# Optimization experiments

Hardware: AMD Instinct MI355X
Metric: run time of the kernel (lower is better)

Reference implementation:

```python
import jax, jax.numpy as jnp
import numpy as np

G, NPG, C, H, F, L = 256, 128, 16, 128, 128, 3
N = G * NPG          # 32768 nodes
E = 524288           # 16 edges per node on average
REG, REG_C = 0.01, 0.01
LN_EPS = 1e-5


def setup_inputs() -> dict:
    key = jax.random.key(0)
    ks = jax.random.split(key, 20)
    x = jax.random.normal(ks[0], (N, F), dtype=jnp.float32)
    # edges kept within each graph so dense pooling matches to_dense_batch semantics
    epg = E // G
    offs = jnp.repeat(jnp.arange(G, dtype=jnp.int64) * NPG, epg)
    src = jax.random.randint(ks[1], (E,), 0, NPG, dtype=jnp.int64) + offs
    tgt = jax.random.randint(ks[2], (E,), 0, NPG, dtype=jnp.int64) + offs
    edge_index = jnp.stack([src, tgt])
    mask_breaks = jax.random.bernoulli(ks[3], 0.5, (E,))
    s = jax.random.uniform(ks[4], (N, C), dtype=jnp.float32)
    batch = jnp.repeat(jnp.arange(G, dtype=jnp.int64), NPG)
    sc = 1.0 / np.sqrt(H)
    Wn = jax.random.normal(ks[5], (L, H, H), dtype=jnp.float32) * sc
    bn_ = jax.random.normal(ks[6], (L, H), dtype=jnp.float32) * sc
    Wo = jax.random.normal(ks[7], (L, H, H), dtype=jnp.float32) * sc
    bo = jax.random.normal(ks[8], (L, H), dtype=jnp.float32) * sc
    Wr = jax.random.normal(ks[9], (L, H, H), dtype=jnp.float32) * sc
    ln_g = jnp.ones((L, H), dtype=jnp.float32)
    ln_b = jnp.zeros((L, H), dtype=jnp.float32)
    fln_g = jnp.ones((H,), dtype=jnp.float32)
    fln_b = jnp.zeros((H,), dtype=jnp.float32)
    lin_w = jax.random.normal(ks[10], (1, H), dtype=jnp.float32) * sc
    bias = jnp.zeros((1,), dtype=jnp.float32)
    return {"x": x, "edge_index": edge_index, "mask_breaks": mask_breaks, "s": s,
            "batch": batch, "Wn": Wn, "bn_": bn_, "Wo": Wo, "bo": bo, "Wr": Wr,
            "ln_g": ln_g, "ln_b": ln_b, "fln_g": fln_g, "fln_b": fln_b,
            "lin_w": lin_w, "bias": bias}


def _layernorm(h, g, b):
    mu = jnp.mean(h, axis=-1, keepdims=True)
    v = jnp.mean(jnp.square(h - mu), axis=-1, keepdims=True)
    return (h - mu) * jax.lax.rsqrt(v + LN_EPS) * g + b


def reference(x, edge_index, mask_breaks, s, batch, Wn, bn_, Wo, bo, Wr,
              ln_g, ln_b, fln_g, fln_b, lin_w, bias):
    src, tgt = edge_index[0], edge_index[1]
    ones_e = jnp.ones((E,), dtype=x.dtype)
    cnt = jax.ops.segment_sum(ones_e, tgt, num_segments=N)          # in-degree
    inv_cnt = (1.0 / jnp.maximum(cnt, 1.0))[:, None]
    h = x
    for i in range(L):
        x_in = h @ Wn[i].T + bn_[i]
        x_out = h @ Wo[i].T + bo[i]
        x_root = h @ Wr[i].T
        msg = jnp.where(mask_breaks[:, None], x_in[src], x_out[src])  # [E,H]
        agg = jax.ops.segment_sum(msg, tgt, num_segments=N) * inv_cnt  # mean aggr
        h = jax.nn.relu(_layernorm(agg + x_root, ln_g[i], ln_b[i]))
    # dense per-graph views (equal-size graphs, batch ids sorted -> reshape)
    xd = h.reshape(G, NPG, H)
    sd = s.reshape(G, NPG, C)
    pooled = jnp.einsum("gnc,gnh->gch", sd, xd)                      # [G,C,H]
    pooled = _layernorm(pooled, fln_g, fln_b)
    xc = pooled @ lin_w.T                                            # [G,C,1]
    col_sum = sd.sum(axis=1)                                          # [G,C]
    cmask = (col_sum > 0)[..., None]
    xc = xc * cmask.astype(xc.dtype)
    out = xc.sum(axis=1) + bias                                      # [G,1]
    reg_loss = jnp.abs(Wo).sum() + jnp.abs(bo).sum()
    denom = (cmask.astype(xc.dtype).squeeze(-1) + 1e-7).sum(axis=1, keepdims=True)
    l1_loss = (jnp.abs(xc).sum(axis=1) / denom).mean()
    losses = REG * reg_loss + REG_C * l1_loss
    return out, losses, xc
```

## Files before the change

### kernel.cpp

```cpp
#include <hip/hip_runtime.h>

#define NN   32768
#define HD   128
#define EE   524288
#define GG   256
#define EPG  2048
#define CCd  16
#define LLd  3

typedef short short8 __attribute__((ext_vector_type(8)));
typedef float f32x4 __attribute__((ext_vector_type(4)));

__device__ __forceinline__ unsigned short f2bf(float f) {
  unsigned u = __builtin_bit_cast(unsigned, f);
  return (unsigned short)((u + 0x7FFFu + ((u >> 16) & 1u)) >> 16);
}
__device__ __forceinline__ unsigned bfpack(float a, float b) {
  return (unsigned)f2bf(a) | ((unsigned)f2bf(b) << 16);
}

__device__ __forceinline__ int hchunk(int f, int c) {
  return f * 128 + (((c ^ ((f ^ (f >> 2)) & 15)) & 15) << 3);
}
__device__ __forceinline__ int hidx(int f, int t) {
  return hchunk(f, t >> 3) + (t & 7);
}

__global__ __launch_bounds__(256) void convert_w_kernel(const float* __restrict__ Wn, const float* __restrict__ Wo,
                                                        const float* __restrict__ Wr, const float* __restrict__ bo,
                                                        unsigned* __restrict__ Wnb, unsigned* __restrict__ Wob,
                                                        unsigned* __restrict__ Wrb, float* __restrict__ wsreg) {
  int i = blockIdx.x * 256 + threadIdx.x;
  float4 a = *(const float4*)(Wn + (size_t)i * 4);
  float4 b = *(const float4*)(Wo + (size_t)i * 4);
  float4 c = *(const float4*)(Wr + (size_t)i * 4);
  *(uint2*)(Wnb + (size_t)i * 2) = make_uint2(bfpack(a.x, a.y), bfpack(a.z, a.w));
  *(uint2*)(Wob + (size_t)i * 2) = make_uint2(bfpack(b.x, b.y), bfpack(b.z, b.w));
  *(uint2*)(Wrb + (size_t)i * 2) = make_uint2(bfpack(c.x, c.y), bfpack(c.z, c.w));
  float s = fabsf(b.x) + fabsf(b.y) + fabsf(b.z) + fabsf(b.w);
  if (blockIdx.x == 0 && threadIdx.x < 96) {
    float4 d = *(const float4*)(bo + threadIdx.x * 4);
    s += fabsf(d.x) + fabsf(d.y) + fabsf(d.z) + fabsf(d.w);
  }
#pragma unroll
  for (int mk = 1; mk < 64; mk <<= 1) s += __shfl_xor(s, mk, 64);
  if ((threadIdx.x & 63) == 0) atomicAdd(wsreg, s);
}

__global__ __launch_bounds__(512) void fused_kernel(
    const float* __restrict__ x,
    const int* __restrict__ esrc, const int* __restrict__ etgt, const int* __restrict__ emask,
    const unsigned short* __restrict__ Wnb, const unsigned short* __restrict__ Wob,
    const unsigned short* __restrict__ Wrb,
    const float* __restrict__ bn, const float* __restrict__ bo,
    const float* __restrict__ lng, const float* __restrict__ lnb,
    const float* __restrict__ s,
    const float* __restrict__ flng, const float* __restrict__ flnb,
    const float* __restrict__ linw, const float* __restrict__ bias,
    float* __restrict__ out, float* __restrict__ l1g) {
  __shared__ __align__(16) unsigned short hTs[128 * 128];
  __shared__ __align__(16) unsigned short sTs[16 * 136];
  __shared__ __align__(16) unsigned Mlds[2 * 128 * 64];
  __shared__ __align__(16) unsigned Wlds[128 * 64];
  __shared__ float finS[128], foutS[128];
  __shared__ float colsumS[CCd], xcs[CCd], axcs[CCd], msk[CCd];

  const int g = blockIdx.x;
  const int tid = threadIdx.x;
  const int wave = tid >> 6;
  const int lane = tid & 63;
  const int m = lane & 15;
  const int q = lane >> 4;
  const int t0 = wave << 4;

  auto w_stage = [&](const unsigned short* __restrict__ Wg) {
#pragma unroll
    for (int c = 0; c < 4; ++c) {
      int row = c * 32 + wave * 4 + (lane >> 4);
      int lc = (lane & 15) ^ (row & 15);
      const unsigned short* gp = Wg + row * 128 + lc * 8;
      unsigned* lp = Wlds + c * 2048 + wave * 256;
      __builtin_amdgcn_global_load_lds(
          (const __attribute__((address_space(1))) unsigned*)gp,
          (__attribute__((address_space(3))) unsigned*)lp, 16, 0, 0);
    }
  };
  auto wfrag = [&](int ct, int ksg) -> short8 {
    return *(const short8*)&Wlds[(ct * 16 + m) * 64 + ((((ksg * 4 + q) ^ m) & 15) << 2)];
  };

  w_stage(Wnb);
  int et[4], es[4], em[4];
  {
    const int e0 = g * EPG;
#pragma unroll
    for (int i = 0; i < 4; ++i) {
      int e = e0 + i * 512 + tid;
      et[i] = etgt[e]; es[i] = esrc[e]; em[i] = emask[e];
    }
  }

  {
    uint4* cz = (uint4*)Mlds;
#pragma unroll
    for (int i = 0; i < 8; ++i) cz[i * 512 + tid] = make_uint4(0u, 0u, 0u, 0u);

    const float4* xg = (const float4*)(x + (size_t)g * 16384);
#pragma unroll
    for (int i = 0; i < 8; ++i) {
      int flat = i * 512 + tid;
      int t = flat >> 5, f0 = (flat & 31) << 2;
      float4 v = xg[flat];
      hTs[hidx(f0 + 0, t)] = f2bf(v.x);
      hTs[hidx(f0 + 1, t)] = f2bf(v.y);
      hTs[hidx(f0 + 2, t)] = f2bf(v.z);
      hTs[hidx(f0 + 3, t)] = f2bf(v.w);
    }
    {
      int t = tid >> 2, c0 = (tid & 3) << 2;
      float4 v = *(const float4*)(s + (size_t)g * 2048 + t * 16 + c0);
      sTs[(c0 + 0) * 136 + t] = f2bf(v.x);
      sTs[(c0 + 1) * 136 + t] = f2bf(v.y);
      sTs[(c0 + 2) * 136 + t] = f2bf(v.z);
      sTs[(c0 + 3) * 136 + t] = f2bf(v.w);
    }
    if (tid < 64) {
      int c = tid & 15, qq = tid >> 4;
      float cs = 0.f;
      for (int tt = qq; tt < 128; tt += 4) cs += s[(size_t)g * 2048 + tt * 16 + c];
      cs += __shfl_xor(cs, 16); cs += __shfl_xor(cs, 32);
      if (qq == 0) colsumS[c] = cs;
    }
  }
  __syncthreads();

  {
#pragma unroll
    for (int i = 0; i < 4; ++i) {
      int t = et[i] & 127;
      int sl = es[i] & 127;
      int dir = (em[i] != 0) ? 0 : 1;
      atomicAdd(&Mlds[dir * 8192 + t * 64 + ((((sl >> 3) ^ (t & 15)) & 15) << 2) + ((sl >> 1) & 3)],
                1u << ((sl & 1) * 16));
    }
  }
  __syncthreads();

  {
    const int t = t0 + m;
    unsigned nin = 0, nout = 0;
#pragma unroll
    for (int k4 = 0; k4 < 4; ++k4) {
      int sl = (((q * 4 + k4) ^ m) & 15) << 2;
      uint4 a = *(const uint4*)&Mlds[t * 64 + sl];
      uint4 b = *(const uint4*)&Mlds[8192 + t * 64 + sl];
      nin  += (a.x & 0xffffu) + (a.x >> 16) + (a.y & 0xffffu) + (a.y >> 16)
            + (a.z & 0xffffu) + (a.z >> 16) + (a.w & 0xffffu) + (a.w >> 16);
      nout += (b.x & 0xffffu) + (b.x >> 16) + (b.y & 0xffffu) + (b.y >> 16)
            + (b.z & 0xffffu) + (b.z >> 16) + (b.w & 0xffffu) + (b.w >> 16);
    }
    nin  += __shfl_xor((int)nin, 16);  nin  += __shfl_xor((int)nin, 32);
    nout += __shfl_xor((int)nout, 16); nout += __shfl_xor((int)nout, 32);
    unsigned dg = nin + nout;
    float inv = 1.0f / (float)(dg > 0 ? dg : 1);
    if (q == 0) { finS[t] = (float)nin * inv; foutS[t] = (float)nout * inv; }
#pragma unroll
    for (int d = 0; d < 2; ++d)
#pragma unroll
      for (int k4 = 0; k4 < 4; ++k4) {
        int sl = (((q * 4 + k4) ^ m) & 15) << 2;
        unsigned* p = &Mlds[d * 8192 + t * 64 + sl];
        uint4 v = *(const uint4*)p;
        uint4 o;
        o.x = bfpack((float)(v.x & 0xffffu) * inv, (float)(v.x >> 16) * inv);
        o.y = bfpack((float)(v.y & 0xffffu) * inv, (float)(v.y >> 16) * inv);
        o.z = bfpack((float)(v.z & 0xffffu) * inv, (float)(v.z >> 16) * inv);
        o.w = bfpack((float)(v.w & 0xffffu) * inv, (float)(v.w >> 16) * inv);
        *(uint4*)p = o;
      }
  }
  __syncthreads();

  for (int L = 0; L < LLd; ++L) {
    const bool more = (L < LLd - 1);
    f32x4 pre[8];
#pragma unroll
    for (int ct = 0; ct < 8; ++ct) pre[ct] = (f32x4){0.f, 0.f, 0.f, 0.f};
    f32x4 accT[8];

#pragma unroll
    for (int ft = 0; ft < 8; ++ft) accT[ft] = (f32x4){0.f, 0.f, 0.f, 0.f};
#pragma unroll
    for (int ksg = 0; ksg < 4; ++ksg) {
      short8 bfr = *(const short8*)&Mlds[(t0 + m) * 64 + ((((ksg * 4 + q) ^ m) & 15) << 2)];
#pragma unroll
      for (int ft = 0; ft < 8; ++ft) {
        short8 afr = *(const short8*)&hTs[hchunk(ft * 16 + m, ksg * 4 + q)];
        accT[ft] = __builtin_amdgcn_mfma_f32_16x16x32_bf16(afr, bfr, accT[ft], 0, 0, 0);
      }
    }
#pragma unroll
    for (int ksg = 0; ksg < 4; ++ksg) {
      f32x4 lo = accT[2 * ksg], hi = accT[2 * ksg + 1];
      unsigned pk[4];
#pragma unroll
      for (int r = 0; r < 4; ++r) pk[r] = bfpack(lo[r], hi[r]);
      short8 afr;
#pragma unroll
      for (int j = 0; j < 8; ++j) {
        int srcl = ((((q & 1) << 1) + (j >> 2)) << 4) + m;
        unsigned v = (unsigned)__shfl((int)pk[j & 3], srcl, 64);
        afr[j] = (short)(unsigned short)((q >> 1) ? (v >> 16) : (v & 0xffffu));
      }
#pragma unroll
      for (int ct = 0; ct < 8; ++ct)
        pre[ct] = __builtin_amdgcn_mfma_f32_16x16x32_bf16(afr, wfrag(ct, ksg), pre[ct], 0, 0, 0);
    }
    __syncthreads();
    w_stage(Wob + L * 16384);

#pragma unroll
    for (int ft = 0; ft < 8; ++ft) accT[ft] = (f32x4){0.f, 0.f, 0.f, 0.f};
#pragma unroll
    for (int ksg = 0; ksg < 4; ++ksg) {
      short8 bfr = *(const short8*)&Mlds[8192 + (t0 + m) * 64 + ((((ksg * 4 + q) ^ m) & 15) << 2)];
#pragma unroll
      for (int ft = 0; ft < 8; ++ft) {
        short8 afr = *(const short8*)&hTs[hchunk(ft * 16 + m, ksg * 4 + q)];
        accT[ft] = __builtin_amdgcn_mfma_f32_16x16x32_bf16(afr, bfr, accT[ft], 0, 0, 0);
      }
    }
    __syncthreads();
#pragma unroll
    for (int ksg = 0; ksg < 4; ++ksg) {
      f32x4 lo = accT[2 * ksg], hi = accT[2 * ksg + 1];
      unsigned pk[4];
#pragma unroll
      for (int r = 0; r < 4; ++r) pk[r] = bfpack(lo[r], hi[r]);
      short8 afr;
#pragma unroll
      for (int j = 0; j < 8; ++j) {
        int srcl = ((((q & 1) << 1) + (j >> 2)) << 4) + m;
        unsigned v = (unsigned)__shfl((int)pk[j & 3], srcl, 64);
        afr[j] = (short)(unsigned short)((q >> 1) ? (v >> 16) : (v & 0xffffu));
      }
#pragma unroll
      for (int ct = 0; ct < 8; ++ct)
        pre[ct] = __builtin_amdgcn_mfma_f32_16x16x32_bf16(afr, wfrag(ct, ksg), pre[ct], 0, 0, 0);
    }
    __syncthreads();
    w_stage(Wrb + L * 16384);
    short8 wra0, wra1, wra2, wra3;
    {
#pragma unroll
      for (int j = 0; j < 8; ++j) {
        wra0[j] = (short)hTs[hidx(0 * 32 + q * 8 + j, t0 + m)];
        wra1[j] = (short)hTs[hidx(1 * 32 + q * 8 + j, t0 + m)];
        wra2[j] = (short)hTs[hidx(2 * 32 + q * 8 + j, t0 + m)];
        wra3[j] = (short)hTs[hidx(3 * 32 + q * 8 + j, t0 + m)];
      }
    }
    __syncthreads();
#pragma unroll
    for (int ct = 0; ct < 8; ++ct) {
      pre[ct] = __builtin_amdgcn_mfma_f32_16x16x32_bf16(wra0, wfrag(ct, 0), pre[ct], 0, 0, 0);
      pre[ct] = __builtin_amdgcn_mfma_f32_16x16x32_bf16(wra1, wfrag(ct, 1), pre[ct], 0, 0, 0);
      pre[ct] = __builtin_amdgcn_mfma_f32_16x16x32_bf16(wra2, wfrag(ct, 2), pre[ct], 0, 0, 0);
      pre[ct] = __builtin_amdgcn_mfma_f32_16x16x32_bf16(wra3, wfrag(ct, 3), pre[ct], 0, 0, 0);
    }
    __syncthreads();
    if (more) w_stage(Wnb + (L + 1) * 16384);

    {
      float fiv[4], fov[4];
#pragma unroll
      for (int r = 0; r < 4; ++r) { fiv[r] = finS[t0 + q * 4 + r]; fov[r] = foutS[t0 + q * 4 + r]; }
#pragma unroll
      for (int ct2 = 0; ct2 < 8; ct2 += 4) {
        float bn4[4], bo4[4];
#pragma unroll
        for (int cc = 0; cc < 4; ++cc) {
          int c = L * 128 + (ct2 + cc) * 16 + m;
          bn4[cc] = bn[c]; bo4[cc] = bo[c];
        }
#pragma unroll
        for (int cc = 0; cc < 4; ++cc)
#pragma unroll
          for (int r = 0; r < 4; ++r)
            pre[ct2 + cc][r] += fiv[r] * bn4[cc] + fov[r] * bo4[cc];
      }
      float gv[8], bv[8];
#pragma unroll
      for (int ct = 0; ct < 8; ++ct) {
        int c = L * 128 + ct * 16 + m;
        gv[ct] = lng[c]; bv[ct] = lnb[c];
      }
#pragma unroll
      for (int r = 0; r < 4; ++r) {
        const int tl = q * 4 + r;
        float sum = 0.f;
#pragma unroll
        for (int ct = 0; ct < 8; ++ct) sum += pre[ct][r];
        sum += __shfl_xor(sum, 1); sum += __shfl_xor(sum, 2);
        sum += __shfl_xor(sum, 4); sum += __shfl_xor(sum, 8);
        const float mu = sum * (1.0f / 128.0f);
        float sq = 0.f;
#pragma unroll
        for (int ct = 0; ct < 8; ++ct) { float d = pre[ct][r] - mu; sq += d * d; }
        sq += __shfl_xor(sq, 1); sq += __shfl_xor(sq, 2);
        sq += __shfl_xor(sq, 4); sq += __shfl_xor(sq, 8);
        const float rstd = rsqrtf(sq * (1.0f / 128.0f) + 1e-5f);
#pragma unroll
        for (int ct = 0; ct < 8; ++ct) {
          float o = fmaxf((pre[ct][r] - mu) * rstd * gv[ct] + bv[ct], 0.0f);
          hTs[hidx(ct * 16 + m, t0 + tl)] = f2bf(o);
        }
      }
    }
    __syncthreads();
  }

  f32x4 pl = (f32x4){0.f, 0.f, 0.f, 0.f};
#pragma unroll
  for (int ks = 0; ks < 4; ++ks) {
    short8 a = *(const short8*)&sTs[m * 136 + ks * 32 + q * 8];
    short8 b = *(const short8*)&hTs[hchunk(wave * 16 + m, ks * 4 + q)];
    pl = __builtin_amdgcn_mfma_f32_16x16x32_bf16(a, b, pl, 0, 0, 0);
  }
  float* pooledS = (float*)Mlds;
#pragma unroll
  for (int r = 0; r < 4; ++r) pooledS[(q * 4 + r) * 132 + wave * 16 + m] = pl[r];
  __syncthreads();

  if (tid < 256) {
    const int c = tid >> 4;
    const int j0 = (tid & 15) << 3;
    float v[8];
#pragma unroll
    for (int jj = 0; jj < 8; ++jj) v[jj] = pooledS[c * 132 + j0 + jj];
    float sum = 0.f;
#pragma unroll
    for (int jj = 0; jj < 8; ++jj) sum += v[jj];
#pragma unroll
    for (int mk = 1; mk < 16; mk <<= 1) sum += __shfl_xor(sum, mk, 64);
    float mu = sum * (1.0f / 128.0f);
    float sq = 0.f;
#pragma unroll
    for (int jj = 0; jj < 8; ++jj) { float d = v[jj] - mu; sq += d * d; }
#pragma unroll
    for (int mk = 1; mk < 16; mk <<= 1) sq += __shfl_xor(sq, mk, 64);
    float rstd = rsqrtf(sq * (1.0f / 128.0f) + 1e-5f);
    float dot = 0.f;
#pragma unroll
    for (int jj = 0; jj < 8; ++jj) {
      float nv = (v[jj] - mu) * rstd * flng[j0 + jj] + flnb[j0 + jj];
      dot += nv * linw[j0 + jj];
    }
#pragma unroll
    for (int mk = 1; mk < 16; mk <<= 1) dot += __shfl_xor(dot, mk, 64);
    if ((tid & 15) == 0) {
      float cm = (colsumS[c] > 0.f) ? 1.0f : 0.0f;
      float xcv = dot * cm;
      out[257 + g * CCd + c] = xcv;
      xcs[c] = xcv; axcs[c] = fabsf(xcv); msk[c] = cm;
    }
  }
  __syncthreads();
  if (tid == 0) {
    float so = 0.f, sa = 0.f, sd = 0.f;
#pragma unroll
    for (int k = 0; k < CCd; ++k) { so += xcs[k]; sa += axcs[k]; sd += msk[k] + 1e-7f; }
    out[g] = so + bias[0];
    l1g[g] = sa / sd;
  }
}

__global__ __launch_bounds__(256) void combine_kernel(const float* __restrict__ l1g, const float* __restrict__ wsreg,
                                                      float* __restrict__ outp) {
  const int tid = threadIdx.x;
  float s2 = l1g[tid];
#pragma unroll
  for (int mk = 1; mk < 64; mk <<= 1) s2 += __shfl_xor(s2, mk, 64);
  __shared__ float rs2[4];
  if ((tid & 63) == 0) rs2[tid >> 6] = s2;
  __syncthreads();
  if (tid == 0) {
    float l1 = (rs2[0] + rs2[1] + rs2[2] + rs2[3]) * (1.0f / GG);
    outp[0] = 0.01f * wsreg[0] + 0.01f * l1;
  }
}

extern "C" void kernel_launch(void* const* d_in, const int* in_sizes, int n_in,
                              void* d_out, int out_size, void* d_ws, size_t ws_size,
                              hipStream_t stream) {
  (void)in_sizes; (void)n_in; (void)out_size; (void)ws_size;
  const float* x    = (const float*)d_in[0];
  const int*   ei   = (const int*)d_in[1];
  const int*   mask = (const int*)d_in[2];
  const float* s    = (const float*)d_in[3];
  const float* Wn   = (const float*)d_in[5];
  const float* bn   = (const float*)d_in[6];
  const float* Wo   = (const float*)d_in[7];
  const float* bo   = (const float*)d_in[8];
  const float* Wr   = (const float*)d_in[9];
  const float* lng  = (const float*)d_in[10];
  const float* lnb  = (const float*)d_in[11];
  const float* flng = (const float*)d_in[12];
  const float* flnb = (const float*)d_in[13];
  const float* linw = (const float*)d_in[14];
  const float* bias = (const float*)d_in[15];
  float* out = (float*)d_out;

  char* ws = (char*)d_ws;
  size_t off = 0;
  auto alloc = [&](size_t b) { char* p = ws + off; off += (b + 255) & ~(size_t)255; return p; };
  unsigned short* Wnb = (unsigned short*)alloc((size_t)LLd * HD * HD * 2);
  unsigned short* Wob = (unsigned short*)alloc((size_t)LLd * HD * HD * 2);
  unsigned short* Wrb = (unsigned short*)alloc((size_t)LLd * HD * HD * 2);
  float* l1g    = (float*)alloc((size_t)GG * 4);
  float* wsreg  = (float*)alloc(256);

  const int* srcA = ei;
  const int* tgtA = ei + EE;

  hipMemsetAsync(wsreg, 0, 4, stream);
  convert_w_kernel<<<LLd * HD * HD / (256 * 4), 256, 0, stream>>>(Wn, Wo, Wr, bo,
      (unsigned*)Wnb, (unsigned*)Wob, (unsigned*)Wrb, wsreg);
  fused_kernel<<<GG, 512, 0, stream>>>(x, srcA, tgtA, mask, Wnb, Wob, Wrb, bn, bo,
                                       lng, lnb, s, flng, flnb, linw, bias, out, l1g);
  combine_kernel<<<1, 256, 0, stream>>>(l1g, wsreg, out + 256);
}
```

Measured before the change: 136.4 us.

## Reorder per-layer GEMMs root-first and overlap weight staging with aggregation MFMAs

Reorders each layer so the root-weight product runs first, followed by the two aggregation-then-weight products in a shared loop. Each weight-tile global-to-LDS load is issued one stage earlier, so it overlaps the aggregation MFMAs (adjacency times h) that do not read the weight buffer. The bf16 rounding routine is swapped for the library __float2bfloat16 intrinsic. The goal is to hide weight-load latency behind compute. The barrier structure changes and needs careful checking for LDS reuse hazards.

```diff
diff --git a/kernel.cpp b/kernel.cpp
--- a/kernel.cpp
+++ b/kernel.cpp
@@ -1,4 +1,5 @@
 #include <hip/hip_runtime.h>
+#include <hip/hip_bf16.h>
 
 #define NN   32768
 #define HD   128
@@ -12,8 +13,7 @@
 typedef float f32x4 __attribute__((ext_vector_type(4)));
 
 __device__ __forceinline__ unsigned short f2bf(float f) {
-  unsigned u = __builtin_bit_cast(unsigned, f);
-  return (unsigned short)((u + 0x7FFFu + ((u >> 16) & 1u)) >> 16);
+  return __builtin_bit_cast(unsigned short, __float2bfloat16(f));
 }
 __device__ __forceinline__ unsigned bfpack(float a, float b) {
   return (unsigned)f2bf(a) | ((unsigned)f2bf(b) << 16);
@@ -89,7 +89,7 @@
     return *(const short8*)&Wlds[(ct * 16 + m) * 64 + ((((ksg * 4 + q) ^ m) & 15) << 2)];
   };
 
-  w_stage(Wnb);
+  w_stage(Wrb);
   int et[4], es[4], em[4];
   {
     const int e0 = g * EPG;
@@ -188,70 +188,8 @@
     for (int ct = 0; ct < 8; ++ct) pre[ct] = (f32x4){0.f, 0.f, 0.f, 0.f};
     f32x4 accT[8];
 
-#pragma unroll
-    for (int ft = 0; ft < 8; ++ft) accT[ft] = (f32x4){0.f, 0.f, 0.f, 0.f};
-#pragma unroll
-    for (int ksg = 0; ksg < 4; ++ksg) {
-      short8 bfr = *(const short8*)&Mlds[(t0 + m) * 64 + ((((ksg * 4 + q) ^ m) & 15) << 2)];
-#pragma unroll
-      for (int ft = 0; ft < 8; ++ft) {
-        short8 afr = *(const short8*)&hTs[hchunk(ft * 16 + m, ksg * 4 + q)];
-        accT[ft] = __builtin_amdgcn_mfma_f32_16x16x32_bf16(afr, bfr, accT[ft], 0, 0, 0);
-      }
-    }
-#pragma unroll
-    for (int ksg = 0; ksg < 4; ++ksg) {
-      f32x4 lo = accT[2 * ksg], hi = accT[2 * ksg + 1];
-      unsigned pk[4];
-#pragma unroll
-      for (int r = 0; r < 4; ++r) pk[r] = bfpack(lo[r], hi[r]);
-      short8 afr;
-#pragma unroll
-      for (int j = 0; j < 8; ++j) {
-        int srcl = ((((q & 1) << 1) + (j >> 2)) << 4) + m;
-        unsigned v = (unsigned)__shfl((int)pk[j & 3], srcl, 64);
-        afr[j] = (short)(unsigned short)((q >> 1) ? (v >> 16) : (v & 0xffffu));
-      }
-#pragma unroll
-      for (int ct = 0; ct < 8; ++ct)
-        pre[ct] = __builtin_amdgcn_mfma_f32_16x16x32_bf16(afr, wfrag(ct, ksg), pre[ct], 0, 0, 0);
-    }
-    __syncthreads();
-    w_stage(Wob + L * 16384);
-
-#pragma unroll
-    for (int ft = 0; ft < 8; ++ft) accT[ft] = (f32x4){0.f, 0.f, 0.f, 0.f};
-#pragma unroll
-    for (int ksg = 0; ksg < 4; ++ksg) {
-      short8 bfr = *(const short8*)&Mlds[8192 + (t0 + m) * 64 + ((((ksg * 4 + q) ^ m) & 15) << 2)];
-#pragma unroll
-      for (int ft = 0; ft < 8; ++ft) {
-        short8 afr = *(const short8*)&hTs[hchunk(ft * 16 + m, ksg * 4 + q)];
-        accT[ft] = __builtin_amdgcn_mfma_f32_16x16x32_bf16(afr, bfr, accT[ft], 0, 0, 0);
-      }
-    }
-    __syncthreads();
-#pragma unroll
-    for (int ksg = 0; ksg < 4; ++ksg) {
-      f32x4 lo = accT[2 * ksg], hi = accT[2 * ksg + 1];
-      unsigned pk[4];
-#pragma unroll
-      for (int r = 0; r < 4; ++r) pk[r] = bfpack(lo[r], hi[r]);
-      short8 afr;
-#pragma unroll
-      for (int j = 0; j < 8; ++j) {
-        int srcl = ((((q & 1) << 1) + (j >> 2)) << 4) + m;
-        unsigned v = (unsigned)__shfl((int)pk[j & 3], srcl, 64);
-        afr[j] = (short)(unsigned short)((q >> 1) ? (v >> 16) : (v & 0xffffu));
-      }
-#pragma unroll
-      for (int ct = 0; ct < 8; ++ct)
-        pre[ct] = __builtin_amdgcn_mfma_f32_16x16x32_bf16(afr, wfrag(ct, ksg), pre[ct], 0, 0, 0);
-    }
-    __syncthreads();
-    w_stage(Wrb + L * 16384);
-    short8 wra0, wra1, wra2, wra3;
     {
+      short8 wra0, wra1, wra2, wra3;
 #pragma unroll
       for (int j = 0; j < 8; ++j) {
         wra0[j] = (short)hTs[hidx(0 * 32 + q * 8 + j, t0 + m)];
@@ -259,17 +197,57 @@
         wra2[j] = (short)hTs[hidx(2 * 32 + q * 8 + j, t0 + m)];
         wra3[j] = (short)hTs[hidx(3 * 32 + q * 8 + j, t0 + m)];
       }
+#pragma unroll
+      for (int ct = 0; ct < 8; ++ct) {
+        pre[ct] = __builtin_amdgcn_mfma_f32_16x16x32_bf16(wra0, wfrag(ct, 0), pre[ct], 0, 0, 0);
+        pre[ct] = __builtin_amdgcn_mfma_f32_16x16x32_bf16(wra1, wfrag(ct, 1), pre[ct], 0, 0, 0);
+        pre[ct] = __builtin_amdgcn_mfma_f32_16x16x32_bf16(wra2, wfrag(ct, 2), pre[ct], 0, 0, 0);
+        pre[ct] = __builtin_amdgcn_mfma_f32_16x16x32_bf16(wra3, wfrag(ct, 3), pre[ct], 0, 0, 0);
+      }
     }
     __syncthreads();
-#pragma unroll
-    for (int ct = 0; ct < 8; ++ct) {
-      pre[ct] = __builtin_amdgcn_mfma_f32_16x16x32_bf16(wra0, wfrag(ct, 0), pre[ct], 0, 0, 0);
-      pre[ct] = __builtin_amdgcn_mfma_f32_16x16x32_bf16(wra1, wfrag(ct, 1), pre[ct], 0, 0, 0);
-      pre[ct] = __builtin_amdgcn_mfma_f32_16x16x32_bf16(wra2, wfrag(ct, 2), pre[ct], 0, 0, 0);
-      pre[ct] = __builtin_amdgcn_mfma_f32_16x16x32_bf16(wra3, wfrag(ct, 3), pre[ct], 0, 0, 0);
-    }
-    __syncthreads();
-    if (more) w_stage(Wnb + (L + 1) * 16384);
+    w_stage(Wnb + L * 16384);
+
+#pragma unroll
+    for (int sg = 0; sg < 2; ++sg) {
+#pragma unroll
+      for (int ft = 0; ft < 8; ++ft) accT[ft] = (f32x4){0.f, 0.f, 0.f, 0.f};
+#pragma unroll
+      for (int ksg = 0; ksg < 4; ++ksg) {
+        short8 bfr = *(const short8*)&Mlds[sg * 8192 + (t0 + m) * 64 + ((((ksg * 4 + q) ^ m) & 15) << 2)];
+#pragma unroll
+        for (int ft = 0; ft < 8; ++ft) {
+          short8 afr = *(const short8*)&hTs[hchunk(ft * 16 + m, ksg * 4 + q)];
+          accT[ft] = __builtin_amdgcn_mfma_f32_16x16x32_bf16(afr, bfr, accT[ft], 0, 0, 0);
+        }
+      }
+      short8 afrs[4];
+#pragma unroll
+      for (int ksg = 0; ksg < 4; ++ksg) {
+        f32x4 lo = accT[2 * ksg], hi = accT[2 * ksg + 1];
+        unsigned pk[4];
+#pragma unroll
+        for (int r = 0; r < 4; ++r) pk[r] = bfpack(lo[r], hi[r]);
+#pragma unroll
+        for (int j = 0; j < 8; ++j) {
+          int srcl = ((((q & 1) << 1) + (j >> 2)) << 4) + m;
+          unsigned v = (unsigned)__shfl((int)pk[j & 3], srcl, 64);
+          afrs[ksg][j] = (short)(unsigned short)((q >> 1) ? (v >> 16) : (v & 0xffffu));
+        }
+      }
+      __syncthreads();
+#pragma unroll
+      for (int ksg = 0; ksg < 4; ++ksg)
+#pragma unroll
+        for (int ct = 0; ct < 8; ++ct)
+          pre[ct] = __builtin_amdgcn_mfma_f32_16x16x32_bf16(afrs[ksg], wfrag(ct, ksg), pre[ct], 0, 0, 0);
+      __syncthreads();
+      if (sg == 0) {
+        w_stage(Wob + L * 16384);
+      } else if (more) {
+        w_stage(Wrb + (L + 1) * 16384);
+      }
+    }
 
     {
       float fiv[4], fov[4];
```

After: 136.3 us. About the same (-0.1%).
